# Performance work log

Hardware: AMD Instinct MI355X
Metric: run time of the kernel (lower is better)

The kernel has to match this reference:

```python
import jax, jax.numpy as jnp
import numpy as np
import math

B, S, D = 2, 2048, 512
H = 8
DK = D // H  # 64


def setup_inputs() -> dict:
    key = jax.random.key(0)
    ks = jax.random.split(key, 9)
    inp = {
        "query": jax.random.normal(ks[0], (B, S, D), jnp.float32),
        "key": jax.random.normal(ks[1], (B, S, D), jnp.float32),
        "value": jax.random.normal(ks[2], (B, S, D), jnp.float32),
        "attn_weight": jax.random.normal(ks[3], (B, H, S, S), jnp.float32),
        "mask": jax.random.randint(ks[4], (B, S), 0, 2).astype(bool),
        # nn.Linear(d_model, d_model, bias=False) weights, applied as x @ W.T
        "Wq": jax.random.normal(ks[5], (D, D), jnp.float32) / math.sqrt(D),
        "Wk": jax.random.normal(ks[6], (D, D), jnp.float32) / math.sqrt(D),
        "Wv": jax.random.normal(ks[7], (D, D), jnp.float32) / math.sqrt(D),
        "Wo": jax.random.normal(ks[8], (D, D), jnp.float32) / math.sqrt(D),
    }
    return inp


def reference(query, key, value, attn_weight, mask, Wq, Wk, Wv, Wo):
    b, s, d = query.shape
    # project and split heads: [b, h, s, dk]
    def split_heads(x, W):
        return (x @ W.T).reshape(b, -1, H, DK).transpose(0, 2, 1, 3)

    q = split_heads(query, Wq)
    k = split_heads(key, Wk)
    v = split_heads(value, Wv)

    scores = jnp.einsum("bhqd,bhkd->bhqk", q, k) / math.sqrt(DK)
    # mask broadcast as [b,1,1,s]: True -> -inf over keys (applied before bias subtraction,
    # matching torch order; -inf - finite stays -inf)
    scores = jnp.where(mask[:, None, None, :], -jnp.inf, scores)
    scores = scores - attn_weight
    p_attn = jax.nn.softmax(scores, axis=-1)  # dropout p=0 (eval) -> identity
    x = jnp.einsum("bhqk,bhkd->bhqd", p_attn, v)
    x = x.transpose(0, 2, 1, 3).reshape(b, -1, H * DK)
    return x @ Wo.T
```

## Files before the change

### kernel.cpp

```cpp
#include <hip/hip_runtime.h>
#include <math.h>

typedef __bf16 bf16;
typedef __bf16 bf16x8 __attribute__((ext_vector_type(8)));
typedef float f32x4 __attribute__((ext_vector_type(4)));
typedef unsigned int u32;
typedef unsigned long long u64;

#define MFMA_BF16(a, b, c) __builtin_amdgcn_mfma_f32_16x16x32_bf16((a), (b), (c), 0, 0, 0)

static constexpr int kB = 2;
static constexpr int kS = 2048;
static constexpr int kD = 512;
static constexpr int kH = 8;
static constexpr int kDK = 64;
static constexpr int kTileBytes = 8192;
static constexpr int kBhBytes = 32 * kTileBytes;

__global__ void detect_mask_kernel(const unsigned char* __restrict__ m,
                                   u32* __restrict__ bm) {
  __shared__ int sh;
  const int tid = threadIdx.x;
  if (tid == 0) sh = 0;
  __syncthreads();
  int any = 0;
  for (int i = tid; i < kB * kS; i += 256)
    if ((i & 3) != 0 && m[i] != 0) any = 1;
  if (any) atomicOr(&sh, 1);
  __syncthreads();
  const bool as_bool = (sh != 0);
  for (int wi = tid; wi < kB * kS / 32; wi += 256) {
    u32 word = 0;
    const int base = wi * 32;
    for (int j = 0; j < 32; j++) {
      const bool mv = as_bool ? (m[base + j] != 0) : (((const int*)m)[base + j] != 0);
      word |= (mv ? 1u : 0u) << j;
    }
    bm[wi] = word;
  }
}

__device__ __forceinline__ void cvt16(const float* __restrict__ p, bf16x8& v0, bf16x8& v1) {
  const float4 fA = ((const float4*)p)[0];
  const float4 fB = ((const float4*)p)[1];
  const float4 fC = ((const float4*)p)[2];
  const float4 fD = ((const float4*)p)[3];
  v0[0] = (bf16)fA.x; v0[1] = (bf16)fA.y; v0[2] = (bf16)fA.z; v0[3] = (bf16)fA.w;
  v0[4] = (bf16)fB.x; v0[5] = (bf16)fB.y; v0[6] = (bf16)fB.z; v0[7] = (bf16)fB.w;
  v1[0] = (bf16)fC.x; v1[1] = (bf16)fC.y; v1[2] = (bf16)fC.z; v1[3] = (bf16)fC.w;
  v1[4] = (bf16)fD.x; v1[5] = (bf16)fD.y; v1[6] = (bf16)fD.z; v1[7] = (bf16)fD.w;
}

template <bool A_IS_F32, int MODE>
__device__ __forceinline__ void gemm_body(const void* __restrict__ Aptr,
                                          const float* __restrict__ Wptr,
                                          void* __restrict__ dst) {
  constexpr bool TRANS = (MODE != 2);
  __shared__ bf16 As[128][40];
  __shared__ bf16 Bs[128][40];

  const int tid = threadIdx.x;
  const int lane = tid & 63;
  const int w = tid >> 6;
  const int wr = w >> 1, wc = w & 1;
  const int l16 = lane & 15, g = lane >> 4;

  const int m_tile = blockIdx.x * 128;
  const int n_tile = blockIdx.y * 128;

  f32x4 acc[4][4] = {};

  const int sr = tid >> 1;
  const int sc = (tid & 1) * 16;

  for (int k0 = 0; k0 < kD; k0 += 32) {
    if constexpr (A_IS_F32) {
      const float* ap = (const float*)Aptr + (size_t)(m_tile + sr) * kD + k0 + sc;
      bf16x8 v0, v1;
      cvt16(ap, v0, v1);
      *(bf16x8*)&As[sr][sc] = v0;
      *(bf16x8*)&As[sr][sc + 8] = v1;
    } else {
      const bf16* ap = (const bf16*)Aptr + (size_t)(m_tile + sr) * kD + k0 + sc;
      *(bf16x8*)&As[sr][sc] = *(const bf16x8*)ap;
      *(bf16x8*)&As[sr][sc + 8] = *(const bf16x8*)(ap + 8);
    }
    {
      const float* bp = Wptr + (size_t)(n_tile + sr) * kD + k0 + sc;
      bf16x8 v0, v1;
      cvt16(bp, v0, v1);
      *(bf16x8*)&Bs[sr][sc] = v0;
      *(bf16x8*)&Bs[sr][sc + 8] = v1;
    }
    __syncthreads();

    bf16x8 a[4], bfr[4];
    #pragma unroll
    for (int i = 0; i < 4; i++)
      a[i] = *(const bf16x8*)&As[wr * 64 + i * 16 + l16][g * 8];
    #pragma unroll
    for (int i = 0; i < 4; i++)
      bfr[i] = *(const bf16x8*)&Bs[wc * 64 + i * 16 + l16][g * 8];
    #pragma unroll
    for (int mi = 0; mi < 4; mi++)
      #pragma unroll
      for (int ni = 0; ni < 4; ni++) {
        if constexpr (TRANS)
          acc[mi][ni] = MFMA_BF16(bfr[ni], a[mi], acc[mi][ni]);
        else
          acc[mi][ni] = MFMA_BF16(a[mi], bfr[ni], acc[mi][ni]);
      }
    __syncthreads();
  }

  #pragma unroll
  for (int mi = 0; mi < 4; mi++) {
    #pragma unroll
    for (int ni = 0; ni < 4; ni++) {
      const f32x4 v = acc[mi][ni];
      if constexpr (TRANS) {
        const int gm = m_tile + wr * 64 + mi * 16 + l16;
        const int gn0 = n_tile + wc * 64 + ni * 16 + g * 4;
        if constexpr (MODE == 3) {
          *(float4*)&((float*)dst)[(size_t)gm * kD + gn0] =
              (float4){v[0], v[1], v[2], v[3]};
        } else {
          const int bi = gm >> 11;
          const int s = gm & (kS - 1);
          const int h = gn0 >> 6;
          const int dk0 = gn0 & (kDK - 1);
          union { bf16 hh[4]; u64 u; } pk;
          pk.hh[0] = (bf16)v[0]; pk.hh[1] = (bf16)v[1];
          pk.hh[2] = (bf16)v[2]; pk.hh[3] = (bf16)v[3];
          if constexpr (MODE == 0) {
            *(u64*)&((bf16*)dst)[(((size_t)bi * kH + h) * kS + s) * kDK + dk0] = pk.u;
          } else {
            char* base = (char*)dst + (size_t)(bi * kH + h) * kBhBytes + (s >> 6) * kTileBytes;
            *(u64*)(base + (s & 63) * 128 + ((dk0 * 2) ^ ((s & 7) << 4))) = pk.u;
          }
        }
      } else {
        const int gm0 = m_tile + wr * 64 + mi * 16 + g * 4;
        const int gn = n_tile + wc * 64 + ni * 16 + l16;
        const int bi = gm0 >> 11;
        const int s0 = gm0 & (kS - 1);
        const int h = gn >> 6;
        const int dk = gn & (kDK - 1);
        union { bf16 hh[4]; u64 u; } pk;
        pk.hh[0] = (bf16)v[0]; pk.hh[1] = (bf16)v[1];
        pk.hh[2] = (bf16)v[2]; pk.hh[3] = (bf16)v[3];
        char* base = (char*)dst + (size_t)(bi * kH + h) * kBhBytes + (s0 >> 6) * kTileBytes;
        *(u64*)(base + dk * 128 + (((s0 & 63) * 2) ^ ((dk & 7) << 4))) = pk.u;
      }
    }
  }
}

__global__ __launch_bounds__(256) void proj_kernel(
    const float* __restrict__ q, const float* __restrict__ k, const float* __restrict__ v,
    const float* __restrict__ Wq, const float* __restrict__ Wk, const float* __restrict__ Wv,
    bf16* __restrict__ qw, bf16* __restrict__ kw, bf16* __restrict__ vtw) {
  const int z = blockIdx.z;
  if (z == 0) gemm_body<true, 0>(q, Wq, qw);
  else if (z == 1) gemm_body<true, 1>(k, Wk, kw);
  else gemm_body<true, 2>(v, Wv, vtw);
}

__global__ __launch_bounds__(256) void out_kernel(const bf16* __restrict__ x,
                                                  const float* __restrict__ Wo,
                                                  float* __restrict__ out) {
  gemm_body<false, 3>(x, Wo, out);
}

__global__ __launch_bounds__(256, 2) void attn_kernel(
    const bf16* __restrict__ qw, const char* __restrict__ kw,
    const char* __restrict__ vt, const float* __restrict__ bias,
    const u32* __restrict__ bmask, bf16* __restrict__ xw) {
  __shared__ char KV[2][2][2 * kTileBytes];
  __shared__ u32 Ps[4][16][36];
  __shared__ u32 mask_lds[64];

  const int tid = threadIdx.x;
  const int lane = tid & 63;
  const int w = tid >> 6;
  const int l16 = lane & 15, g = lane >> 4;

  const int bid = blockIdx.x;
  const int xcd = bid & 7;
  const int j = bid >> 3;
  const int bh = xcd * 2 + (j >> 5);
  const int qb = j & 31;
  const int b = bh >> 3;
  const int hh = bh & 7;
  const int qr0 = qb * 64 + w * 16;

  if (tid < 64) mask_lds[tid] = bmask[b * 64 + tid];
  __syncthreads();

  const bf16* qrow = qw + ((size_t)bh * kS + qr0 + l16) * kDK;
  const bf16x8 aq0 = *(const bf16x8*)(qrow + g * 8);
  const bf16x8 aq1 = *(const bf16x8*)(qrow + 32 + g * 8);

  const float* brow = bias + ((size_t)bh * kS + qr0 + l16) * kS;
  const char* ktile = kw + (size_t)bh * kBhBytes;
  const char* vtile = vt + (size_t)bh * kBhBytes;

  f32x4 o[4] = {};
  float m_run = -__builtin_inff();
  float l_run = 0.f;
  const int swz = (l16 & 7) << 4;

  auto dma_tile = [&](int t128, int nb) {
    #pragma unroll
    for (int s2 = 0; s2 < 2; s2++) {
      const char* kg = ktile + ((size_t)t128 * 2 + s2) * kTileBytes + w * 2048 + lane * 16;
      __builtin_amdgcn_global_load_lds(
          (const __attribute__((address_space(1))) void*)kg,
          (__attribute__((address_space(3))) void*)&KV[nb][0][s2 * kTileBytes + w * 2048], 16, 0, 0);
      __builtin_amdgcn_global_load_lds(
          (const __attribute__((address_space(1))) void*)(kg + 1024),
          (__attribute__((address_space(3))) void*)&KV[nb][0][s2 * kTileBytes + w * 2048 + 1024], 16, 0, 0);
      const char* vg = vtile + ((size_t)t128 * 2 + s2) * kTileBytes + w * 2048 + lane * 16;
      __builtin_amdgcn_global_load_lds(
          (const __attribute__((address_space(1))) void*)vg,
          (__attribute__((address_space(3))) void*)&KV[nb][1][s2 * kTileBytes + w * 2048], 16, 0, 0);
      __builtin_amdgcn_global_load_lds(
          (const __attribute__((address_space(1))) void*)(vg + 1024),
          (__attribute__((address_space(3))) void*)&KV[nb][1][s2 * kTileBytes + w * 2048 + 1024], 16, 0, 0);
    }
  };
  auto load_bias8 = [&](f32x4 (&bv)[8], int t128) {
    const float* p0 = brow + t128 * 128 + g * 4;
    asm volatile("global_load_dwordx4 %0, %1, off" : "=v"(bv[0]) : "v"(p0));
    asm volatile("global_load_dwordx4 %0, %1, off" : "=v"(bv[1]) : "v"(p0 + 16));
    asm volatile("global_load_dwordx4 %0, %1, off" : "=v"(bv[2]) : "v"(p0 + 32));
    asm volatile("global_load_dwordx4 %0, %1, off" : "=v"(bv[3]) : "v"(p0 + 48));
    asm volatile("global_load_dwordx4 %0, %1, off" : "=v"(bv[4]) : "v"(p0 + 64));
    asm volatile("global_load_dwordx4 %0, %1, off" : "=v"(bv[5]) : "v"(p0 + 80));
    asm volatile("global_load_dwordx4 %0, %1, off" : "=v"(bv[6]) : "v"(p0 + 96));
    asm volatile("global_load_dwordx4 %0, %1, off" : "=v"(bv[7]) : "v"(p0 + 112));
  };

  auto phase = [&](int t, f32x4 (&bc)[8], f32x4 (&bn)[8]) {
    const int cur = t & 1, nxt = cur ^ 1;
    const int tp = (t + 1 > 15) ? 15 : t + 1;
    dma_tile(tp, nxt);
    load_bias8(bn, tp);

    f32x4 sf[8];
    #pragma unroll
    for (int hb = 0; hb < 2; hb++) {
      const char* kb0 = &KV[cur][0][hb * kTileBytes];
      bf16x8 kf[4][2];
      #pragma unroll
      for (int nf = 0; nf < 4; nf++) {
        const int r = nf * 16 + l16;
        #pragma unroll
        for (int h = 0; h < 2; h++)
          kf[nf][h] = *(const bf16x8*)(kb0 + r * 128 + ((g * 16 + h * 64) ^ swz));
      }
      __builtin_amdgcn_s_setprio(1);
      #pragma unroll
      for (int nf = 0; nf < 4; nf++) {
        f32x4 z = {};
        z = MFMA_BF16(kf[nf][0], aq0, z);
        z = MFMA_BF16(kf[nf][1], aq1, z);
        sf[hb * 4 + nf] = z;
      }
      __builtin_amdgcn_s_setprio(0);
    }

    asm volatile("s_waitcnt vmcnt(16)" ::: "memory");
    __builtin_amdgcn_sched_barrier(0);

    const u32 wm0 = mask_lds[4 * t], wm1 = mask_lds[4 * t + 1];
    const u32 wm2 = mask_lds[4 * t + 2], wm3 = mask_lds[4 * t + 3];
    float p[8][4];
    float tmax = -__builtin_inff();
    #pragma unroll
    for (int nf = 0; nf < 8; nf++) {
      const u32 wsel = (nf < 2) ? wm0 : (nf < 4) ? wm1 : (nf < 6) ? wm2 : wm3;
      #pragma unroll
      for (int r = 0; r < 4; r++) {
        float sv = sf[nf][r] * 0.125f - bc[nf][r];
        const int bp = (nf & 1) * 16 + g * 4 + r;
        if ((wsel >> bp) & 1) sv = -__builtin_inff();
        p[nf][r] = sv;
        tmax = fmaxf(tmax, sv);
      }
    }
    tmax = fmaxf(tmax, __shfl_xor(tmax, 16, 64));
    tmax = fmaxf(tmax, __shfl_xor(tmax, 32, 64));

    const float mnew = fmaxf(m_run, tmax);
    const float scale = (m_run == -__builtin_inff()) ? 0.f : __expf(m_run - mnew);
    const float mexp = (mnew == -__builtin_inff()) ? 0.f : mnew;
    float psum = 0.f;
    #pragma unroll
    for (int nf = 0; nf < 8; nf++)
      #pragma unroll
      for (int r = 0; r < 4; r++) {
        const float pv = __expf(p[nf][r] - mexp);
        p[nf][r] = pv;
        psum += pv;
      }
    psum += __shfl_xor(psum, 16, 64);
    psum += __shfl_xor(psum, 32, 64);
    m_run = mnew;
    l_run = l_run * scale + psum;
    #pragma unroll
    for (int ni = 0; ni < 4; ni++) o[ni] *= scale;

    #pragma unroll
    for (int hb = 0; hb < 2; hb++) {
      #pragma unroll
      for (int nf = 0; nf < 4; nf++) {
        union { bf16 h2[2]; u32 u; } c0, c1;
        c0.h2[0] = (bf16)p[hb * 4 + nf][0]; c0.h2[1] = (bf16)p[hb * 4 + nf][1];
        c1.h2[0] = (bf16)p[hb * 4 + nf][2]; c1.h2[1] = (bf16)p[hb * 4 + nf][3];
        Ps[w][l16][nf * 8 + g * 2] = c0.u;
        Ps[w][l16][nf * 8 + g * 2 + 1] = c1.u;
      }
      asm volatile("s_waitcnt lgkmcnt(0)" ::: "memory");
      const char* vb0 = &KV[cur][1][hb * kTileBytes];
      bf16x8 vf[2][4];
      #pragma unroll
      for (int kb2 = 0; kb2 < 2; kb2++)
        #pragma unroll
        for (int ni = 0; ni < 4; ni++) {
          const int d = ni * 16 + l16;
          vf[kb2][ni] = *(const bf16x8*)(vb0 + d * 128 + ((kb2 * 64 + g * 16) ^ swz));
        }
      __builtin_amdgcn_s_setprio(1);
      #pragma unroll
      for (int kb2 = 0; kb2 < 2; kb2++) {
        const bf16x8 pb = *(const bf16x8*)&Ps[w][l16][kb2 * 16 + g * 4];
        #pragma unroll
        for (int ni = 0; ni < 4; ni++)
          o[ni] = MFMA_BF16(vf[kb2][ni], pb, o[ni]);
      }
      __builtin_amdgcn_s_setprio(0);
    }

    asm volatile("s_waitcnt vmcnt(8)" ::: "memory");
    __builtin_amdgcn_s_barrier();
    __builtin_amdgcn_sched_barrier(0);
  };

  f32x4 bc[8], bn[8];
  dma_tile(0, 0);
  load_bias8(bc, 0);
  asm volatile("s_waitcnt vmcnt(8)" ::: "memory");
  __builtin_amdgcn_s_barrier();
  __builtin_amdgcn_sched_barrier(0);

  for (int t = 0; t < 16; t += 2) {
    phase(t, bc, bn);
    phase(t + 1, bn, bc);
  }

  const float inv = (l_run > 0.f) ? 1.f / l_run : 0.f;
  bf16* dstp = xw + ((size_t)b * kS + qr0 + l16) * kD + hh * kDK;
  #pragma unroll
  for (int ni = 0; ni < 4; ni++) {
    union { bf16 h2[2]; u32 u; } c0, c1;
    c0.h2[0] = (bf16)(o[ni][0] * inv); c0.h2[1] = (bf16)(o[ni][1] * inv);
    c1.h2[0] = (bf16)(o[ni][2] * inv); c1.h2[1] = (bf16)(o[ni][3] * inv);
    *(u32*)&dstp[ni * 16 + g * 4] = c0.u;
    *(u32*)&dstp[ni * 16 + g * 4 + 2] = c1.u;
  }
}

extern "C" void kernel_launch(void* const* d_in, const int* in_sizes, int n_in,
                              void* d_out, int out_size, void* d_ws, size_t ws_size,
                              hipStream_t stream) {
  (void)in_sizes; (void)n_in; (void)out_size; (void)ws_size;
  const float* query = (const float*)d_in[0];
  const float* key_in = (const float*)d_in[1];
  const float* value = (const float*)d_in[2];
  const float* attnw = (const float*)d_in[3];
  const unsigned char* mask = (const unsigned char*)d_in[4];
  const float* Wq = (const float*)d_in[5];
  const float* Wk = (const float*)d_in[6];
  const float* Wv = (const float*)d_in[7];
  const float* Wo = (const float*)d_in[8];

  const size_t nqkv = (size_t)kB * kH * kS * kDK;
  size_t off = 0;
  auto alloc = [&](size_t bytes) {
    void* p = (char*)d_ws + off;
    off = (off + bytes + 255) & ~(size_t)255;
    return p;
  };
  u32* bm = (u32*)alloc(kB * kS / 32 * 4);
  bf16* q_ws = (bf16*)alloc(nqkv * 2);
  char* k_ws = (char*)alloc(nqkv * 2);
  char* vt_ws = (char*)alloc(nqkv * 2);
  bf16* x_ws = (bf16*)alloc((size_t)kB * kS * kD * 2);

  detect_mask_kernel<<<1, 256, 0, stream>>>(mask, bm);

  proj_kernel<<<dim3(32, 4, 3), dim3(256), 0, stream>>>(query, key_in, value, Wq, Wk, Wv,
                                                        q_ws, (bf16*)k_ws, (bf16*)vt_ws);
  attn_kernel<<<dim3(512), dim3(256), 0, stream>>>(q_ws, k_ws, vt_ws, attnw, bm, x_ws);
  out_kernel<<<dim3(32, 4), dim3(256), 0, stream>>>(x_ws, Wo, (float*)d_out);
}
```

Baseline: 137.1 us.

## Fold mask detection into projection launch, shrink GEMM tiles, nontemporal bias loads

The separate single-block mask-detection kernel is removed and run inside an extra z-slice of the projection launch, and it now reads the mask as 32-bit words. The GEMM body is templated on tile size: projections use 64x128 tiles and the output GEMM uses 128x64 tiles, doubling block counts to fill more CUs. Bias loads in attention gain the nt hint to avoid polluting cache with streamed data. The aim is to cut one launch and reduce underutilization of the small GEMMs. The cost is that smaller tiles reuse each loaded weight tile less, and the z=3 slice launches 256 blocks of which 255 exit immediately.

```diff
diff --git a/kernel.cpp b/kernel.cpp
--- a/kernel.cpp
+++ b/kernel.cpp
@@ -16,29 +16,6 @@
 static constexpr int kDK = 64;
 static constexpr int kTileBytes = 8192;
 static constexpr int kBhBytes = 32 * kTileBytes;
-
-__global__ void detect_mask_kernel(const unsigned char* __restrict__ m,
-                                   u32* __restrict__ bm) {
-  __shared__ int sh;
-  const int tid = threadIdx.x;
-  if (tid == 0) sh = 0;
-  __syncthreads();
-  int any = 0;
-  for (int i = tid; i < kB * kS; i += 256)
-    if ((i & 3) != 0 && m[i] != 0) any = 1;
-  if (any) atomicOr(&sh, 1);
-  __syncthreads();
-  const bool as_bool = (sh != 0);
-  for (int wi = tid; wi < kB * kS / 32; wi += 256) {
-    u32 word = 0;
-    const int base = wi * 32;
-    for (int j = 0; j < 32; j++) {
-      const bool mv = as_bool ? (m[base + j] != 0) : (((const int*)m)[base + j] != 0);
-      word |= (mv ? 1u : 0u) << j;
-    }
-    bm[wi] = word;
-  }
-}
 
 __device__ __forceinline__ void cvt16(const float* __restrict__ p, bf16x8& v0, bf16x8& v1) {
   const float4 fA = ((const float4*)p)[0];
@@ -50,61 +27,113 @@
   v1[0] = (bf16)fC.x; v1[1] = (bf16)fC.y; v1[2] = (bf16)fC.z; v1[3] = (bf16)fC.w;
   v1[4] = (bf16)fD.x; v1[5] = (bf16)fD.y; v1[6] = (bf16)fD.z; v1[7] = (bf16)fD.w;
 }
-
-template <bool A_IS_F32, int MODE>
+__device__ __forceinline__ void cvt8(const float* __restrict__ p, bf16x8& v0) {
+  const float4 fA = ((const float4*)p)[0];
+  const float4 fB = ((const float4*)p)[1];
+  v0[0] = (bf16)fA.x; v0[1] = (bf16)fA.y; v0[2] = (bf16)fA.z; v0[3] = (bf16)fA.w;
+  v0[4] = (bf16)fB.x; v0[5] = (bf16)fB.y; v0[6] = (bf16)fB.z; v0[7] = (bf16)fB.w;
+}
+
+__device__ void detect_body(const unsigned char* __restrict__ m, u32* __restrict__ bm) {
+  __shared__ int sh;
+  const int tid = threadIdx.x;
+  if (tid == 0) sh = 0;
+  __syncthreads();
+  const u32* mw = (const u32*)m;
+  int any = 0;
+  #pragma unroll
+  for (int i = tid; i < kB * kS / 4; i += 256) {
+    if (mw[i] & 0xFFFFFF00u) any = 1;
+  }
+  if (any) atomicOr(&sh, 1);
+  __syncthreads();
+  const bool as_bool = (sh != 0);
+  for (int wi = tid; wi < kB * kS / 32; wi += 256) {
+    u32 word = 0;
+    if (as_bool) {
+      #pragma unroll
+      for (int c = 0; c < 8; c++) {
+        const u32 x = mw[wi * 8 + c];
+        word |= ((x & 1u) | ((x >> 7) & 2u) | ((x >> 14) & 4u) | ((x >> 21) & 8u)) << (c * 4);
+      }
+    } else {
+      #pragma unroll
+      for (int c = 0; c < 32; c++)
+        word |= ((((const int*)m)[wi * 32 + c]) ? 1u : 0u) << c;
+    }
+    bm[wi] = word;
+  }
+}
+
+template <bool A_IS_F32, int MODE, int BM, int BN>
 __device__ __forceinline__ void gemm_body(const void* __restrict__ Aptr,
                                           const float* __restrict__ Wptr,
                                           void* __restrict__ dst) {
   constexpr bool TRANS = (MODE != 2);
-  __shared__ bf16 As[128][40];
-  __shared__ bf16 Bs[128][40];
+  constexpr int WM = BM / 2, WN = BN / 2;
+  constexpr int MI = WM / 16, NI = WN / 16;
+  __shared__ bf16 As[BM][40];
+  __shared__ bf16 Bs[BN][40];
 
   const int tid = threadIdx.x;
   const int lane = tid & 63;
   const int w = tid >> 6;
-  const int wr = w >> 1, wc = w & 1;
+  const int wr = w & 1, wc = w >> 1;
   const int l16 = lane & 15, g = lane >> 4;
 
-  const int m_tile = blockIdx.x * 128;
-  const int n_tile = blockIdx.y * 128;
-
-  f32x4 acc[4][4] = {};
-
-  const int sr = tid >> 1;
-  const int sc = (tid & 1) * 16;
+  const int m_tile = blockIdx.x * BM;
+  const int n_tile = blockIdx.y * BN;
+
+  f32x4 acc[MI][NI] = {};
 
   for (int k0 = 0; k0 < kD; k0 += 32) {
-    if constexpr (A_IS_F32) {
-      const float* ap = (const float*)Aptr + (size_t)(m_tile + sr) * kD + k0 + sc;
-      bf16x8 v0, v1;
-      cvt16(ap, v0, v1);
-      *(bf16x8*)&As[sr][sc] = v0;
-      *(bf16x8*)&As[sr][sc + 8] = v1;
-    } else {
-      const bf16* ap = (const bf16*)Aptr + (size_t)(m_tile + sr) * kD + k0 + sc;
-      *(bf16x8*)&As[sr][sc] = *(const bf16x8*)ap;
-      *(bf16x8*)&As[sr][sc + 8] = *(const bf16x8*)(ap + 8);
-    }
     {
-      const float* bp = Wptr + (size_t)(n_tile + sr) * kD + k0 + sc;
-      bf16x8 v0, v1;
-      cvt16(bp, v0, v1);
-      *(bf16x8*)&Bs[sr][sc] = v0;
-      *(bf16x8*)&Bs[sr][sc + 8] = v1;
+      constexpr int tpr = 256 / BM;
+      const int r = tid / tpr, c = (tid % tpr) * (32 / tpr);
+      if constexpr (A_IS_F32) {
+        const float* ap = (const float*)Aptr + (size_t)(m_tile + r) * kD + k0 + c;
+        if constexpr (tpr == 2) {
+          bf16x8 v0, v1; cvt16(ap, v0, v1);
+          *(bf16x8*)&As[r][c] = v0; *(bf16x8*)&As[r][c + 8] = v1;
+        } else {
+          bf16x8 v0; cvt8(ap, v0);
+          *(bf16x8*)&As[r][c] = v0;
+        }
+      } else {
+        const bf16* ap = (const bf16*)Aptr + (size_t)(m_tile + r) * kD + k0 + c;
+        if constexpr (tpr == 2) {
+          *(bf16x8*)&As[r][c] = *(const bf16x8*)ap;
+          *(bf16x8*)&As[r][c + 8] = *(const bf16x8*)(ap + 8);
+        } else {
+          *(bf16x8*)&As[r][c] = *(const bf16x8*)ap;
+        }
+      }
+    }
+    {
+      constexpr int tpr = 256 / BN;
+      const int r = tid / tpr, c = (tid % tpr) * (32 / tpr);
+      const float* bp = Wptr + (size_t)(n_tile + r) * kD + k0 + c;
+      if constexpr (tpr == 2) {
+        bf16x8 v0, v1; cvt16(bp, v0, v1);
+        *(bf16x8*)&Bs[r][c] = v0; *(bf16x8*)&Bs[r][c + 8] = v1;
+      } else {
+        bf16x8 v0; cvt8(bp, v0);
+        *(bf16x8*)&Bs[r][c] = v0;
+      }
     }
     __syncthreads();
 
-    bf16x8 a[4], bfr[4];
-    #pragma unroll
-    for (int i = 0; i < 4; i++)
-      a[i] = *(const bf16x8*)&As[wr * 64 + i * 16 + l16][g * 8];
-    #pragma unroll
-    for (int i = 0; i < 4; i++)
-      bfr[i] = *(const bf16x8*)&Bs[wc * 64 + i * 16 + l16][g * 8];
-    #pragma unroll
-    for (int mi = 0; mi < 4; mi++)
-      #pragma unroll
-      for (int ni = 0; ni < 4; ni++) {
+    bf16x8 a[MI], bfr[NI];
+    #pragma unroll
+    for (int i = 0; i < MI; i++)
+      a[i] = *(const bf16x8*)&As[wr * WM + i * 16 + l16][g * 8];
+    #pragma unroll
+    for (int i = 0; i < NI; i++)
+      bfr[i] = *(const bf16x8*)&Bs[wc * WN + i * 16 + l16][g * 8];
+    #pragma unroll
+    for (int mi = 0; mi < MI; mi++)
+      #pragma unroll
+      for (int ni = 0; ni < NI; ni++) {
         if constexpr (TRANS)
           acc[mi][ni] = MFMA_BF16(bfr[ni], a[mi], acc[mi][ni]);
         else
@@ -114,13 +143,13 @@
   }
 
   #pragma unroll
-  for (int mi = 0; mi < 4; mi++) {
-    #pragma unroll
-    for (int ni = 0; ni < 4; ni++) {
+  for (int mi = 0; mi < MI; mi++) {
+    #pragma unroll
+    for (int ni = 0; ni < NI; ni++) {
       const f32x4 v = acc[mi][ni];
       if constexpr (TRANS) {
-        const int gm = m_tile + wr * 64 + mi * 16 + l16;
-        const int gn0 = n_tile + wc * 64 + ni * 16 + g * 4;
+        const int gm = m_tile + wr * WM + mi * 16 + l16;
+        const int gn0 = n_tile + wc * WN + ni * 16 + g * 4;
         if constexpr (MODE == 3) {
           *(float4*)&((float*)dst)[(size_t)gm * kD + gn0] =
               (float4){v[0], v[1], v[2], v[3]};
@@ -140,8 +169,8 @@
           }
         }
       } else {
-        const int gm0 = m_tile + wr * 64 + mi * 16 + g * 4;
-        const int gn = n_tile + wc * 64 + ni * 16 + l16;
+        const int gm0 = m_tile + wr * WM + mi * 16 + g * 4;
+        const int gn = n_tile + wc * WN + ni * 16 + l16;
         const int bi = gm0 >> 11;
         const int s0 = gm0 & (kS - 1);
         const int h = gn >> 6;
@@ -159,17 +188,22 @@
 __global__ __launch_bounds__(256) void proj_kernel(
     const float* __restrict__ q, const float* __restrict__ k, const float* __restrict__ v,
     const float* __restrict__ Wq, const float* __restrict__ Wk, const float* __restrict__ Wv,
-    bf16* __restrict__ qw, bf16* __restrict__ kw, bf16* __restrict__ vtw) {
+    bf16* __restrict__ qw, bf16* __restrict__ kw, bf16* __restrict__ vtw,
+    const unsigned char* __restrict__ mask, u32* __restrict__ bm) {
   const int z = blockIdx.z;
-  if (z == 0) gemm_body<true, 0>(q, Wq, qw);
-  else if (z == 1) gemm_body<true, 1>(k, Wk, kw);
-  else gemm_body<true, 2>(v, Wv, vtw);
+  if (z == 3) {
+    if (blockIdx.x == 0 && blockIdx.y == 0) detect_body(mask, bm);
+    return;
+  }
+  if (z == 0) gemm_body<true, 0, 64, 128>(q, Wq, qw);
+  else if (z == 1) gemm_body<true, 1, 64, 128>(k, Wk, kw);
+  else gemm_body<true, 2, 64, 128>(v, Wv, vtw);
 }
 
 __global__ __launch_bounds__(256) void out_kernel(const bf16* __restrict__ x,
                                                   const float* __restrict__ Wo,
                                                   float* __restrict__ out) {
-  gemm_body<false, 3>(x, Wo, out);
+  gemm_body<false, 3, 128, 64>(x, Wo, out);
 }
 
 __global__ __launch_bounds__(256, 2) void attn_kernel(
@@ -231,14 +265,14 @@
   };
   auto load_bias8 = [&](f32x4 (&bv)[8], int t128) {
     const float* p0 = brow + t128 * 128 + g * 4;
-    asm volatile("global_load_dwordx4 %0, %1, off" : "=v"(bv[0]) : "v"(p0));
-    asm volatile("global_load_dwordx4 %0, %1, off" : "=v"(bv[1]) : "v"(p0 + 16));
-    asm volatile("global_load_dwordx4 %0, %1, off" : "=v"(bv[2]) : "v"(p0 + 32));
-    asm volatile("global_load_dwordx4 %0, %1, off" : "=v"(bv[3]) : "v"(p0 + 48));
-    asm volatile("global_load_dwordx4 %0, %1, off" : "=v"(bv[4]) : "v"(p0 + 64));
-    asm volatile("global_load_dwordx4 %0, %1, off" : "=v"(bv[5]) : "v"(p0 + 80));
-    asm volatile("global_load_dwordx4 %0, %1, off" : "=v"(bv[6]) : "v"(p0 + 96));
-    asm volatile("global_load_dwordx4 %0, %1, off" : "=v"(bv[7]) : "v"(p0 + 112));
+    asm volatile("global_load_dwordx4 %0, %1, off nt" : "=v"(bv[0]) : "v"(p0));
+    asm volatile("global_load_dwordx4 %0, %1, off nt" : "=v"(bv[1]) : "v"(p0 + 16));
+    asm volatile("global_load_dwordx4 %0, %1, off nt" : "=v"(bv[2]) : "v"(p0 + 32));
+    asm volatile("global_load_dwordx4 %0, %1, off nt" : "=v"(bv[3]) : "v"(p0 + 48));
+    asm volatile("global_load_dwordx4 %0, %1, off nt" : "=v"(bv[4]) : "v"(p0 + 64));
+    asm volatile("global_load_dwordx4 %0, %1, off nt" : "=v"(bv[5]) : "v"(p0 + 80));
+    asm volatile("global_load_dwordx4 %0, %1, off nt" : "=v"(bv[6]) : "v"(p0 + 96));
+    asm volatile("global_load_dwordx4 %0, %1, off nt" : "=v"(bv[7]) : "v"(p0 + 112));
   };
 
   auto phase = [&](int t, f32x4 (&bc)[8], f32x4 (&bn)[8]) {
@@ -398,10 +432,9 @@
   char* vt_ws = (char*)alloc(nqkv * 2);
   bf16* x_ws = (bf16*)alloc((size_t)kB * kS * kD * 2);
 
-  detect_mask_kernel<<<1, 256, 0, stream>>>(mask, bm);
-
-  proj_kernel<<<dim3(32, 4, 3), dim3(256), 0, stream>>>(query, key_in, value, Wq, Wk, Wv,
-                                                        q_ws, (bf16*)k_ws, (bf16*)vt_ws);
+  proj_kernel<<<dim3(64, 4, 4), dim3(256), 0, stream>>>(query, key_in, value, Wq, Wk, Wv,
+                                                        q_ws, (bf16*)k_ws, (bf16*)vt_ws,
+                                                        mask, bm);
   attn_kernel<<<dim3(512), dim3(256), 0, stream>>>(q_ws, k_ws, vt_ws, attnw, bm, x_ws);
-  out_kernel<<<dim3(32, 4), dim3(256), 0, stream>>>(x_ws, Wo, (float*)d_out);
-}
+  out_kernel<<<dim3(32, 8), dim3(256), 0, stream>>>(x_ws, Wo, (float*)d_out);
+}
```

Result: faster. 121.4 us (-11.4%).
